# Optimization experiments

Measured on AMD Instinct MI355X. Metric: run time of the kernel, lower is better.

The kernel has to match this reference:

```python
import jax, jax.numpy as jnp
import numpy as np

N = 50000
E = 1600000
EPS = 1e-16


def transformer_conv(x, src, dst, ea, Wq, bq, Wk, bk, Wv, bv, We, Ws, bs):
    # PyG TransformerConv, heads=1, concat=True, root_weight=True
    C = Wq.shape[1]
    q = x @ Wq + bq                      # [N, C]
    k = x @ Wk + bk                      # [N, C]
    v = x @ Wv + bv                      # [N, C]
    e = ea @ We                          # [E, C]
    k_e = k[src] + e                     # per-edge key
    v_e = v[src] + e                     # per-edge value
    score = (q[dst] * k_e).sum(-1) / jnp.sqrt(jnp.asarray(C, x.dtype))  # [E]
    # segment softmax over incoming edges of each dst node
    m = jax.ops.segment_max(score, dst, num_segments=N)
    ex = jnp.exp(score - m[dst])
    denom = jax.ops.segment_sum(ex, dst, num_segments=N)
    alpha = ex / (denom[dst] + EPS)
    out = jax.ops.segment_sum(alpha[:, None] * v_e, dst, num_segments=N)
    return out + x @ Ws + bs             # skip connection


def gcn_conv(x, src, dst, W, b):
    # PyG GCNConv: self-loops + symmetric deg^-1/2 normalization
    n_idx = jnp.arange(N)
    src2 = jnp.concatenate([src, n_idx])
    dst2 = jnp.concatenate([dst, n_idx])
    deg = jax.ops.segment_sum(jnp.ones(E + N, x.dtype), dst2, num_segments=N)
    dinv = jnp.where(deg > 0, jax.lax.rsqrt(deg), 0.0)
    norm = dinv[src2] * dinv[dst2]       # [E+N]
    h = x @ W                            # [N, out]
    out = jax.ops.segment_sum(norm[:, None] * h[src2], dst2, num_segments=N)
    return out + b


def setup_inputs() -> dict:
    key = jax.random.key(0)
    ks = jax.random.split(key, 32)
    d = {}
    d['x'] = jax.random.normal(ks[0], (N, 128), jnp.float32)
    d['edge_index'] = jax.random.randint(ks[1], (2, E), 0, N, jnp.int64)
    d['edge_attr'] = jax.random.normal(ks[2], (E, 16), jnp.float32)
    shapes = dict(
        Wq1=(128, 96), bq1=(96,), Wk1=(128, 96), bk1=(96,), Wv1=(128, 96), bv1=(96,),
        We1=(16, 96), Ws1=(128, 96), bs1=(96,),
        Wq2=(96, 64), bq2=(64,), Wk2=(96, 64), bk2=(64,), Wv2=(96, 64), bv2=(64,),
        We2=(16, 64), Ws2=(96, 64), bs2=(64,),
        Wmu=(64, 32), bmu=(32,), Wls=(64, 32), bls=(32,))
    for i, (name, shp) in enumerate(shapes.items()):
        scale = 1.0 / np.sqrt(shp[0]) if len(shp) == 2 else 0.02
        d[name] = jax.random.normal(ks[3 + i], shp, jnp.float32) * scale
    return d


def reference(x, edge_index, edge_attr,
              Wq1, bq1, Wk1, bk1, Wv1, bv1, We1, Ws1, bs1,
              Wq2, bq2, Wk2, bk2, Wv2, bv2, We2, Ws2, bs2,
              Wmu, bmu, Wls, bls):
    src, dst = edge_index[0], edge_index[1]
    h = jax.nn.relu(transformer_conv(x, src, dst, edge_attr,
                                     Wq1, bq1, Wk1, bk1, Wv1, bv1, We1, Ws1, bs1))
    h = jax.nn.relu(transformer_conv(h, src, dst, edge_attr,
                                     Wq2, bq2, Wk2, bk2, Wv2, bv2, We2, Ws2, bs2))
    mu = gcn_conv(h, src, dst, Wmu, bmu)
    logstd = gcn_conv(h, src, dst, Wls, bls)
    return mu, logstd
```

## Files before the change

kernel.cpp:

```cpp
#include <hip/hip_runtime.h>
#include <math.h>


#define TPB 256
#define NGRP 8
typedef unsigned int uint32;
typedef unsigned long long u64;
typedef unsigned short u16;
typedef __attribute__((ext_vector_type(4))) float f32x4;
typedef __attribute__((ext_vector_type(4))) uint32 u32x4;
typedef __attribute__((ext_vector_type(4))) int i32x4;
typedef __attribute__((ext_vector_type(8))) short bf16x8;

__device__ __forceinline__ uint32 f2bf(float f) {
    uint32 u = __float_as_uint(f);
    return (u + 0x7fffu + ((u >> 16) & 1u)) >> 16;
}
__device__ __forceinline__ float bf2f(uint32 b) { return __uint_as_float(b << 16); }

__global__ void hist_kernel(const int* __restrict__ dst, int* __restrict__ deg,
                            int E, int span) {
    int grp = blockIdx.x & (NGRP - 1);
    int lo = grp * span;
    int nb = gridDim.x >> 3;
    int bid = blockIdx.x >> 3;
    int stride = nb * TPB * 8;
    for (int base = (bid * TPB + threadIdx.x) * 8; base < E; base += stride) {
        if (base + 8 <= E) {
            i32x4 d0 = __builtin_nontemporal_load((const i32x4*)(dst + base));
            i32x4 d1 = __builtin_nontemporal_load((const i32x4*)(dst + base + 4));
            int dv[8] = {d0.x, d0.y, d0.z, d0.w, d1.x, d1.y, d1.z, d1.w};
#pragma unroll
            for (int u = 0; u < 8; ++u)
                if ((uint32)(dv[u] - lo) < (uint32)span) atomicAdd(&deg[dv[u]], 1);
        } else {
            for (int i = base; i < E; ++i) {
                int d = dst[i];
                if ((uint32)(d - lo) < (uint32)span) atomicAdd(&deg[d], 1);
            }
        }
    }
}

__global__ __launch_bounds__(1024) void scan1_kernel(const int* __restrict__ deg,
                                                     int* __restrict__ prowp,
                                                     int* __restrict__ bsum, int n) {
    __shared__ int wsum[16];
    __shared__ int woff[16];
    int tid = threadIdx.x;
    int i = blockIdx.x * 1024 + tid;
    int lane = tid & 63, w = tid >> 6;
    int dg = (i < n) ? deg[i] : 0;
    int x = (dg + 7) & ~7;
    int v = x;
#pragma unroll
    for (int off = 1; off < 64; off <<= 1) {
        int t = __shfl_up(v, off, 64);
        if (lane >= off) v += t;
    }
    if (lane == 63) wsum[w] = v;
    __syncthreads();
    if (tid < 64) {
        int s = (tid < 16) ? wsum[tid] : 0;
#pragma unroll
        for (int off = 1; off < 16; off <<= 1) {
            int t = __shfl_up(s, off, 64);
            if (lane >= off) s += t;
        }
        if (tid < 16) woff[tid] = s;
    }
    __syncthreads();
    int incl = v + (w ? woff[w - 1] : 0);
    if (i < n) prowp[i] = incl;
    if (tid == 1023) bsum[blockIdx.x] = incl;
}

__global__ void scan2_kernel(const int* __restrict__ bsum, int* __restrict__ boff,
                             int* __restrict__ prowpN, int nb) {
    int tid = threadIdx.x;
    int x = (tid < nb) ? bsum[tid] : 0;
    int v = x;
#pragma unroll
    for (int off = 1; off < 64; off <<= 1) {
        int t = __shfl_up(v, off, 64);
        if (tid >= off) v += t;
    }
    if (tid < nb) boff[tid] = v - x;
    if (tid == nb - 1) *prowpN = v;
}

__global__ __launch_bounds__(1024) void scan3_kernel(const int* __restrict__ deg,
                                                     const int* __restrict__ boff,
                                                     int* __restrict__ prowp,
                                                     int* __restrict__ cursor,
                                                     float* __restrict__ dinv,
                                                     u64* __restrict__ pse, int n) {
    int i = blockIdx.x * 1024 + threadIdx.x;
    if (i < n) {
        int dg = deg[i];
        int x = (dg + 7) & ~7;
        int excl = prowp[i] - x + boff[blockIdx.x];
        prowp[i] = excl;
        cursor[i] = excl;
        dinv[i] = 1.0f / sqrtf((float)(dg + 1));
        u64 pad = (u64)(uint32)n;
        for (int p = excl + dg; p < excl + x; ++p) pse[p] = pad;
    }
}

__global__ void scatter_kernel(const int* __restrict__ src, const int* __restrict__ dst,
                               int* __restrict__ cursor, u64* __restrict__ pse,
                               int E, int span) {
    int grp = blockIdx.x & (NGRP - 1);
    int lo = grp * span;
    int nb = gridDim.x >> 3;
    int bid = blockIdx.x >> 3;
    int stride = nb * TPB * 8;
    for (int base = (bid * TPB + threadIdx.x) * 8; base < E; base += stride) {
        if (base + 8 <= E) {
            i32x4 d0 = __builtin_nontemporal_load((const i32x4*)(dst + base));
            i32x4 d1 = __builtin_nontemporal_load((const i32x4*)(dst + base + 4));
            i32x4 s0 = __builtin_nontemporal_load((const i32x4*)(src + base));
            i32x4 s1 = __builtin_nontemporal_load((const i32x4*)(src + base + 4));
            int dv[8] = {d0.x, d0.y, d0.z, d0.w, d1.x, d1.y, d1.z, d1.w};
            int sv[8] = {s0.x, s0.y, s0.z, s0.w, s1.x, s1.y, s1.z, s1.w};
#pragma unroll
            for (int u = 0; u < 8; ++u) {
                if ((uint32)(dv[u] - lo) < (uint32)span) {
                    int pos = atomicAdd(&cursor[dv[u]], 1);
                    pse[pos] = ((u64)(uint32)(base + u) << 32) | (uint32)sv[u];
                }
            }
        } else {
            for (int i = base; i < E; ++i) {
                int d = dst[i];
                if ((uint32)(d - lo) < (uint32)span) {
                    int pos = atomicAdd(&cursor[d], 1);
                    pse[pos] = ((u64)(uint32)i << 32) | (uint32)src[i];
                }
            }
        }
    }
}

__global__ void permute_kernel(const u64* __restrict__ pse, const float* __restrict__ EA,
                               const int* __restrict__ prowpN,
                               int* __restrict__ psrc, u16* __restrict__ EAb,
                               int N, int cap) {
    int i = blockIdx.x * TPB + threadIdx.x;
    if (i >= cap) return;
    int tot = *prowpN;
    if (i >= tot) return;
    u64 pk = __builtin_nontemporal_load(pse + i);
    uint32 s = (uint32)pk;
    uint32 eid = (uint32)(pk >> 32);
    __builtin_nontemporal_store((int)s, psrc + i);
    u32x4 lo = {0u, 0u, 0u, 0u}, hi = {0u, 0u, 0u, 0u};
    if (s != (uint32)N) {
        const f32x4* e4 = (const f32x4*)(EA + (size_t)eid * 16);
        f32x4 a = __builtin_nontemporal_load(e4);
        f32x4 b = __builtin_nontemporal_load(e4 + 1);
        f32x4 c = __builtin_nontemporal_load(e4 + 2);
        f32x4 d = __builtin_nontemporal_load(e4 + 3);
        lo = (u32x4){f2bf(a.x) | (f2bf(a.y) << 16), f2bf(a.z) | (f2bf(a.w) << 16),
                     f2bf(b.x) | (f2bf(b.y) << 16), f2bf(b.z) | (f2bf(b.w) << 16)};
        hi = (u32x4){f2bf(c.x) | (f2bf(c.y) << 16), f2bf(c.z) | (f2bf(c.w) << 16),
                     f2bf(d.x) | (f2bf(d.y) << 16), f2bf(d.z) | (f2bf(d.w) << 16)};
    }
    u32x4* o = (u32x4*)(EAb + (size_t)i * 16);
    __builtin_nontemporal_store(lo, o);
    __builtin_nontemporal_store(hi, o + 1);
}

__global__ void pack_kernel(
    const float* Wq1, const float* Wk1, const float* Wv1, const float* Ws1,
    const float* bq1, const float* bk1, const float* bv1, const float* bs1,
    const float* We1,
    const float* Wq2, const float* Wk2, const float* Wv2, const float* Ws2,
    const float* bq2, const float* bk2, const float* bv2, const float* bs2,
    const float* We2,
    const float* Wmu, const float* bmu, const float* Wls, const float* bls,
    const float* x, unsigned short* xb, int NX,
    unsigned short* Wc1t, float* bc1, unsigned short* Wc2t, float* bc2,
    float* Wc3, float* bc3) {
    const float s1 = 0.1020620726159658f;
    const float s2 = 0.125f;
    int gi = blockIdx.x * TPB + threadIdx.x;
    const int R0 = 448 * 128, R1 = R0 + 320 * 96, R2 = R1 + 64 * 64;
    const int R3 = R2 + 448, R4 = R3 + 320, R5 = R4 + 64;
    for (int i = gi; i < R5; i += gridDim.x * TPB) {
        if (i < R0) {
            int c = i / 128, kk = i % 128;
            float v = 0.f;
            if (c < 96) v = Wq1[kk * 96 + c] * s1;
            else if (c < 112) {
                int t = c - 96; float a = 0.f;
                for (int u = 0; u < 96; ++u) a += Wq1[kk * 96 + u] * We1[t * 96 + u];
                v = a * s1;
            } else if (c < 304) {
                int tt = c - 112;
                v = (tt & 1) ? Wv1[kk * 96 + (tt >> 1)] : Wk1[kk * 96 + (tt >> 1)];
            } else if (c < 400) v = Ws1[kk * 96 + (c - 304)];
            Wc1t[i] = (unsigned short)f2bf(v);
        } else if (i < R1) {
            int j = i - R0;
            int c = j / 96, kk = j % 96;
            float v = 0.f;
            if (c < 64) v = Wq2[kk * 64 + c] * s2;
            else if (c < 80) {
                int t = c - 64; float a = 0.f;
                for (int u = 0; u < 64; ++u) a += Wq2[kk * 64 + u] * We2[t * 64 + u];
                v = a * s2;
            } else if (c < 208) {
                int tt = c - 80;
                v = (tt & 1) ? Wv2[kk * 64 + (tt >> 1)] : Wk2[kk * 64 + (tt >> 1)];
            } else if (c < 272) v = Ws2[kk * 64 + (c - 208)];
            Wc2t[j] = (unsigned short)f2bf(v);
        } else if (i < R2) {
            int j = i - R1;
            int k = j / 64, c = j % 64;
            Wc3[j] = (c < 32) ? Wmu[k * 32 + c] : Wls[k * 32 + (c - 32)];
        } else if (i < R3) {
            int c = i - R2;
            float v = 0.f;
            if (c < 96) v = bq1[c] * s1;
            else if (c < 112) {
                int t = c - 96; float a = 0.f;
                for (int u = 0; u < 96; ++u) a += bq1[u] * We1[t * 96 + u];
                v = a * s1;
            } else if (c < 304) {
                int tt = c - 112;
                v = (tt & 1) ? bv1[tt >> 1] : bk1[tt >> 1];
            } else if (c < 400) v = bs1[c - 304];
            bc1[c] = v;
        } else if (i < R4) {
            int c = i - R3;
            float v = 0.f;
            if (c < 64) v = bq2[c] * s2;
            else if (c < 80) {
                int t = c - 64; float a = 0.f;
                for (int u = 0; u < 64; ++u) a += bq2[u] * We2[t * 64 + u];
                v = a * s2;
            } else if (c < 208) {
                int tt = c - 80;
                v = (tt & 1) ? bv2[tt >> 1] : bk2[tt >> 1];
            } else if (c < 272) v = bs2[c - 208];
            bc2[c] = v;
        } else {
            int c = i - R4;
            bc3[c] = (c < 32) ? bmu[c] : bls[c - 32];
        }
    }
    for (int i = gi; i < NX; i += gridDim.x * TPB)
        xb[i] = (unsigned short)f2bf(x[i]);
}

__global__ __launch_bounds__(256) void mfma_gemm_kernel(
    const unsigned short* __restrict__ A,
    const unsigned short* __restrict__ Wt,
    const float* __restrict__ bias,
    float* __restrict__ Qs, float* __restrict__ QE,
    uint32* __restrict__ KVp, float* __restrict__ SK,
    int N, int K, int Cq) {
    __shared__ unsigned short As[64][56];
    __shared__ unsigned short Bs[64][56];
    int r0 = blockIdx.x * 64, c0 = blockIdx.y * 64;
    int tid = threadIdx.x;
    int lane = tid & 63, w = tid >> 6;
    int wm = w >> 1, wn = w & 1;
    int l15 = lane & 15, l4 = lane >> 4;
    f32x4 zero = {0.f, 0.f, 0.f, 0.f};
    f32x4 acc[2][2] = {{zero, zero}, {zero, zero}};
    int sr = tid >> 2, sk = (tid & 3) * 8;

    for (int kc = 0; kc < K; kc += 32) {
        bf16x8 av = {};
        int ar = r0 + sr;
        if (ar < N) av = *(const bf16x8*)(A + (size_t)ar * K + kc + sk);
        *(bf16x8*)&As[sr][sk] = av;
        bf16x8 bv = *(const bf16x8*)(Wt + (size_t)(c0 + sr) * K + kc + sk);
        *(bf16x8*)&Bs[sr][sk] = bv;
        __syncthreads();
        bf16x8 af0 = *(const bf16x8*)&As[32 * wm + l15][l4 * 8];
        bf16x8 af1 = *(const bf16x8*)&As[32 * wm + 16 + l15][l4 * 8];
        bf16x8 bf0 = *(const bf16x8*)&Bs[32 * wn + l15][l4 * 8];
        bf16x8 bf1 = *(const bf16x8*)&Bs[32 * wn + 16 + l15][l4 * 8];
        acc[0][0] = __builtin_amdgcn_mfma_f32_16x16x32_bf16(af0, bf0, acc[0][0], 0, 0, 0);
        acc[0][1] = __builtin_amdgcn_mfma_f32_16x16x32_bf16(af0, bf1, acc[0][1], 0, 0, 0);
        acc[1][0] = __builtin_amdgcn_mfma_f32_16x16x32_bf16(af1, bf0, acc[1][0], 0, 0, 0);
        acc[1][1] = __builtin_amdgcn_mfma_f32_16x16x32_bf16(af1, bf1, acc[1][1], 0, 0, 0);
        __syncthreads();
    }

    int qe0 = Cq, kv0 = Cq + 16, sk0 = 3 * Cq + 16, end0 = 4 * Cq + 16;
#pragma unroll
    for (int fm = 0; fm < 2; ++fm) {
#pragma unroll
        for (int fn = 0; fn < 2; ++fn) {
            int cb = c0 + 32 * wn + 16 * fn;
            int c = cb + l15;
            float bia = bias[c];
#pragma unroll
            for (int r = 0; r < 4; ++r) {
                int row = r0 + 32 * wm + 16 * fm + l4 * 4 + r;
                float v = acc[fm][fn][r] + bia;
                float pv = __shfl_xor(v, 1, 64);
                bool ok = row < N;
                if (cb < qe0) {
                    if (ok) Qs[(size_t)row * Cq + c] = v;
                } else if (cb < kv0) {
                    if (ok) QE[(size_t)row * 16 + (c - qe0)] = v;
                } else if (cb < sk0) {
                    if (ok && !(l15 & 1)) {
                        int t = c - kv0;
                        KVp[(size_t)row * Cq + (t >> 1)] = (f2bf(v) << 16) | f2bf(pv);
                    }
                } else if (cb < end0) {
                    if (ok) SK[(size_t)row * Cq + (c - sk0)] = v;
                }
            }
        }
    }
}

template <int C>
__global__ __launch_bounds__(256) void edge_attn_kernel(
    const float* __restrict__ Qs, const float* __restrict__ SK,
    const uint32* __restrict__ KVp,
    const u16* __restrict__ EAb, const float* __restrict__ QE,
    const int* __restrict__ prowp, const int* __restrict__ deg,
    const int* __restrict__ psrc,
    float* __restrict__ Hpre, float* __restrict__ AEA, int N) {
    constexpr int CPL = C / 32;
    int n = blockIdx.x * 4 + (threadIdx.x >> 6);
    if (n >= N) return;
    int lane = threadIdx.x & 63;
    int half = lane >> 5, l = lane & 31, t16 = l & 15;
    bool lo16 = (l < 16);

    uint32 nC = (uint32)n * C;
    float q[CPL], acc[CPL];
#pragma unroll
    for (int j = 0; j < CPL; ++j) { q[j] = Qs[nC + l + 32 * j]; acc[j] = 0.f; }
    float qe = lo16 ? QE[(uint32)n * 16 + t16] : 0.f;
    float d = 0.f, aea = 0.f;
    int eb = prowp[n], ee = prowp[n + 1];

    for (int base = eb + 8 * half; base < ee; base += 16) {
        const int* sp = psrc + base;
        const u16* ep = EAb + (size_t)base * 16 + t16;
        float dots[8], eav[8];
        uint32 kv[8][CPL];
#pragma unroll
        for (int u = 0; u < 8; ++u) {
            int s = __builtin_nontemporal_load(sp + u);
            eav[u] = bf2f(__builtin_nontemporal_load(ep + u * 16));
            uint32 off = (uint32)s * C + l;
            float dt = qe * eav[u];
#pragma unroll
            for (int j = 0; j < CPL; ++j) {
                uint32 t = KVp[off + 32 * j];
                kv[u][j] = t;
                dt = fmaf(q[j], __uint_as_float(t & 0xffff0000u), dt);
            }
            dots[u] = dt;
        }
#pragma unroll
        for (int a = 0; a < 4; ++a) {
            float x0 = dots[2 * a], x1 = dots[2 * a + 1];
            float z = (lo16 ? x0 : x1) + __shfl_xor(lo16 ? x1 : x0, 16, 64);
            z += __shfl_xor(z, 8, 64);
            z += __shfl_xor(z, 4, 64);
            z += __shfl_xor(z, 2, 64);
            z += __shfl_xor(z, 1, 64);
            float p = __expf(z);
            float p0 = __shfl(p, 0, 32);
            float p1 = __shfl(p, 16, 32);
            d += p0 + p1;
            aea = fmaf(p0, eav[2 * a], fmaf(p1, eav[2 * a + 1], aea));
#pragma unroll
            for (int j = 0; j < CPL; ++j)
                acc[j] = fmaf(p0, __uint_as_float(kv[2 * a][j] << 16),
                         fmaf(p1, __uint_as_float(kv[2 * a + 1][j] << 16), acc[j]));
        }
    }
    d += __shfl_xor(d, 32, 64);
    aea += __shfl_xor(aea, 32, 64);
    d -= (float)((ee - eb) - deg[n]);
    float inv = 1.f / (d + 1e-16f);
#pragma unroll
    for (int j = 0; j < CPL; ++j) {
        float a2 = acc[j] + __shfl_xor(acc[j], 32, 64);
        if (half == 0)
            Hpre[nC + l + 32 * j] = a2 * inv + SK[nC + l + 32 * j];
    }
    if (lane < 16) AEA[(uint32)n * 16 + t16] = aea * inv;
}

template <int C>
__global__ void fixup_relu_kernel(const float* __restrict__ Hpre, const float* __restrict__ AEA,
                                  const float* __restrict__ We,
                                  unsigned short* __restrict__ H1b, int NC) {
    int idx = blockIdx.x * TPB + threadIdx.x;
    if (idx >= NC) return;
    int n = idx / C, c = idx % C;
    const float* a = AEA + (size_t)n * 16;
    float s = Hpre[idx];
#pragma unroll
    for (int t = 0; t < 16; ++t) s += a[t] * We[t * C + c];
    H1b[idx] = (unsigned short)f2bf(fmaxf(s, 0.f));
}

__global__ void fixup2_kernel(const float* __restrict__ Hpre, const float* __restrict__ AEA,
                              const float* __restrict__ We, const float* __restrict__ dinv,
                              uint32* __restrict__ H2p, int N) {
    int idx = blockIdx.x * TPB + threadIdx.x;
    if (idx >= N * 32) return;
    int n = idx >> 5, c = idx & 31;
    const float* a = AEA + (size_t)n * 16;
    float s0 = Hpre[(size_t)n * 64 + c];
    float s1 = Hpre[(size_t)n * 64 + 32 + c];
#pragma unroll
    for (int t = 0; t < 16; ++t) {
        s0 += a[t] * We[t * 64 + c];
        s1 += a[t] * We[t * 64 + 32 + c];
    }
    float dn = dinv[n];
    s0 = fmaxf(s0, 0.f) * dn;
    s1 = fmaxf(s1, 0.f) * dn;
    H2p[idx] = f2bf(s0) | (f2bf(s1) << 16);
}

__global__ __launch_bounds__(256) void gcn_agg_kernel(
    const uint32* __restrict__ H2p, const int* __restrict__ prowp,
    const int* __restrict__ psrc, const float* __restrict__ dinv,
    float* __restrict__ AGG, int N) {
    int n = blockIdx.x * 4 + (threadIdx.x >> 6);
    if (n >= N) return;
    int lane = threadIdx.x & 63, half = lane >> 5, l = lane & 31;
    float s0 = 0.f, s1 = 0.f;
    int eb = prowp[n], ee = prowp[n + 1];
    for (int base = eb + 8 * half; base < ee; base += 16) {
        const int* sp = psrc + base;
#pragma unroll
        for (int u = 0; u < 8; ++u) {
            uint32 s = (uint32)__builtin_nontemporal_load(sp + u);
            uint32 t = H2p[s * 32 + l];
            s0 += bf2f(t & 0xffffu);
            s1 += __uint_as_float(t & 0xffff0000u);
        }
    }
    s0 += __shfl_xor(s0, 32, 64);
    s1 += __shfl_xor(s1, 32, 64);
    if (half == 0) {
        uint32 u = H2p[(uint32)n * 32 + l];
        float dn = dinv[n];
        AGG[(uint32)n * 64 + l]      = dn * (s0 + bf2f(u & 0xffffu));
        AGG[(uint32)n * 64 + 32 + l] = dn * (s1 + __uint_as_float(u & 0xffff0000u));
    }
}

template <int CT, bool SPLIT>
__global__ __launch_bounds__(256) void gemm_kernel(
    const float* __restrict__ A, const float* __restrict__ W,
    const float* __restrict__ bias, float* __restrict__ Out,
    float* __restrict__ Out2, int N, int K, int C) {
    constexpr int TC = CT / 16;
    __shared__ float As[32][68];
    __shared__ float Bs[32][CT + 4];
    int r0 = blockIdx.x * 64, c0 = blockIdx.y * CT;
    int t = threadIdx.x;
    int tr = t >> 4, tc = t & 15;
    float acc[4][TC];
#pragma unroll
    for (int i = 0; i < 4; ++i)
#pragma unroll
        for (int j = 0; j < TC; ++j) acc[i][j] = 0.f;

    for (int kc = 0; kc < K; kc += 32) {
        int ra = t >> 2, kq = (t & 3) * 8;
        float4 a0 = {0, 0, 0, 0}, a1 = {0, 0, 0, 0};
        int r = r0 + ra;
        if (r < N) {
            const float* ap = A + (size_t)r * K + kc + kq;
            a0 = *(const float4*)ap;
            a1 = *(const float4*)(ap + 4);
        }
        As[kq + 0][ra] = a0.x; As[kq + 1][ra] = a0.y;
        As[kq + 2][ra] = a0.z; As[kq + 3][ra] = a0.w;
        As[kq + 4][ra] = a1.x; As[kq + 5][ra] = a1.y;
        As[kq + 6][ra] = a1.z; As[kq + 7][ra] = a1.w;
        constexpr int PASSES = (32 * CT) / (256 * 8);
#pragma unroll
        for (int p = 0; p < PASSES; ++p) {
            int idx = (t + p * 256) * 8;
            int k = idx / CT, c = idx % CT;
            const float* wp = W + (size_t)(kc + k) * C + c0 + c;
            float4 b0 = *(const float4*)wp;
            float4 b1 = *(const float4*)(wp + 4);
            *(float4*)&Bs[k][c] = b0;
            *(float4*)&Bs[k][c + 4] = b1;
        }
        __syncthreads();
#pragma unroll
        for (int k = 0; k < 32; ++k) {
            float4 av = *(const float4*)&As[k][tr * 4];
            float a[4] = {av.x, av.y, av.z, av.w};
#pragma unroll
            for (int u = 0; u < TC / 4; ++u) {
                float4 bv = *(const float4*)&Bs[k][tc * TC + u * 4];
                float b[4] = {bv.x, bv.y, bv.z, bv.w};
#pragma unroll
                for (int i = 0; i < 4; ++i)
#pragma unroll
                    for (int j = 0; j < 4; ++j) acc[i][u * 4 + j] += a[i] * b[j];
            }
        }
        __syncthreads();
    }
#pragma unroll
    for (int i = 0; i < 4; ++i) {
        int r = r0 + tr * 4 + i;
        if (r >= N) continue;
#pragma unroll
        for (int j = 0; j < TC; ++j) {
            int c = c0 + tc * TC + j;
            float v = acc[i][j] + bias[c];
            if (SPLIT) {
                if (c < 32) Out[(size_t)r * 32 + c] = v;
                else        Out2[(size_t)r * 32 + c - 32] = v;
            } else {
                Out[(size_t)r * C + c] = v;
            }
        }
    }
}

extern "C" void kernel_launch(void* const* d_in, const int* in_sizes, int n_in,
                              void* d_out, int out_size, void* d_ws, size_t ws_size,
                              hipStream_t stream) {
    const float* x   = (const float*)d_in[0];
    const int*   ei  = (const int*)d_in[1];
    const float* ea  = (const float*)d_in[2];
    const float* Wq1 = (const float*)d_in[3];  const float* bq1 = (const float*)d_in[4];
    const float* Wk1 = (const float*)d_in[5];  const float* bk1 = (const float*)d_in[6];
    const float* Wv1 = (const float*)d_in[7];  const float* bv1 = (const float*)d_in[8];
    const float* We1 = (const float*)d_in[9];
    const float* Ws1 = (const float*)d_in[10]; const float* bs1 = (const float*)d_in[11];
    const float* Wq2 = (const float*)d_in[12]; const float* bq2 = (const float*)d_in[13];
    const float* Wk2 = (const float*)d_in[14]; const float* bk2 = (const float*)d_in[15];
    const float* Wv2 = (const float*)d_in[16]; const float* bv2 = (const float*)d_in[17];
    const float* We2 = (const float*)d_in[18];
    const float* Ws2 = (const float*)d_in[19]; const float* bs2 = (const float*)d_in[20];
    const float* Wmu = (const float*)d_in[21]; const float* bmu = (const float*)d_in[22];
    const float* Wls = (const float*)d_in[23]; const float* bls = (const float*)d_in[24];

    int N = in_sizes[0] / 128;
    int E = in_sizes[1] / 2;
    const int* src = ei;
    const int* dst = ei + E;
    int E2max = E + 8 * N;
    int span = (N + NGRP - 1) / NGRP;

    char* ws = (char*)d_ws;
    size_t off = 0;
    auto alloc = [&](size_t bytes) -> char* {
        char* p = ws + off;
        off = (off + bytes + 255) & ~(size_t)255;
        return p;
    };
    int*      deg    = (int*)alloc((size_t)N * 4);
    int*      prowp  = (int*)alloc((size_t)(N + 1) * 4);
    int*      cursor = (int*)alloc((size_t)N * 4);
    float*    dinv   = (float*)alloc((size_t)N * 4);
    int*      bsum   = (int*)alloc(256 * 4);
    int*      boff   = (int*)alloc(256 * 4);
    u64*      pse    = (u64*)alloc((size_t)E2max * 8);
    int*      psrc   = (int*)alloc((size_t)E2max * 4);
    u16*      EAb    = (u16*)alloc((size_t)E2max * 16 * 2);
    unsigned short* Wc1t = (unsigned short*)alloc(448 * 128 * 2);
    float*    bc1    = (float*)alloc(448 * 4);
    unsigned short* Wc2t = (unsigned short*)alloc(320 * 96 * 2);
    float*    bc2    = (float*)alloc(320 * 4);
    float*    Wc3    = (float*)alloc(64 * 64 * 4);
    float*    bc3    = (float*)alloc(64 * 4);
    unsigned short* xb = (unsigned short*)alloc((size_t)N * 128 * 2);
    float*    Qs   = (float*)alloc((size_t)N * 96 * 4);
    float*    QE   = (float*)alloc((size_t)N * 16 * 4);
    uint32*   KVp  = (uint32*)alloc((size_t)(N + 1) * 96 * 4);
    float*    SKb  = (float*)alloc((size_t)N * 96 * 4);
    float*    Hpre = (float*)alloc((size_t)N * 96 * 4);
    unsigned short* H1b = (unsigned short*)alloc((size_t)N * 96 * 2);
    float*    AEA  = (float*)alloc((size_t)N * 16 * 4);
    uint32*   H2p  = (uint32*)alloc((size_t)(N + 1) * 32 * 4);
    float*    AGG  = (float*)alloc((size_t)N * 64 * 4);

    (void)hipMemsetAsync(deg, 0, (size_t)N * 4, stream);
    (void)hipMemsetAsync(KVp + (size_t)N * 96, 0, 96 * 4, stream);
    (void)hipMemsetAsync(H2p + (size_t)N * 32, 0, 32 * 4, stream);

    int e2bk = (E2max + TPB - 1) / TPB;
    int nb1k = (N + 1023) / 1024;
    hist_kernel<<<2048, TPB, 0, stream>>>(dst, deg, E, span);
    scan1_kernel<<<nb1k, 1024, 0, stream>>>(deg, prowp, bsum, N);
    scan2_kernel<<<1, 64, 0, stream>>>(bsum, boff, prowp + N, nb1k);
    scan3_kernel<<<nb1k, 1024, 0, stream>>>(deg, boff, prowp, cursor, dinv, pse, N);
    scatter_kernel<<<2048, TPB, 0, stream>>>(src, dst, cursor, pse, E, span);
    permute_kernel<<<e2bk, TPB, 0, stream>>>(pse, ea, prowp + N, psrc, EAb, N, E2max);
    pack_kernel<<<364, TPB, 0, stream>>>(Wq1, Wk1, Wv1, Ws1, bq1, bk1, bv1, bs1, We1,
                                         Wq2, Wk2, Wv2, Ws2, bq2, bk2, bv2, bs2, We2,
                                         Wmu, bmu, Wls, bls, x, xb, N * 128,
                                         Wc1t, bc1, Wc2t, bc2, Wc3, bc3);

    int rb = (N + 63) / 64;
    int nb4 = (N + 3) / 4;

    mfma_gemm_kernel<<<dim3(rb, 7), 256, 0, stream>>>(xb, Wc1t, bc1, Qs, QE, KVp, SKb,
                                                      N, 128, 96);
    edge_attn_kernel<96><<<nb4, 256, 0, stream>>>(Qs, SKb, KVp, EAb, QE, prowp, deg, psrc,
                                                  Hpre, AEA, N);
    fixup_relu_kernel<96><<<(N * 96 + TPB - 1) / TPB, TPB, 0, stream>>>(Hpre, AEA, We1,
                                                                        H1b, N * 96);
    mfma_gemm_kernel<<<dim3(rb, 5), 256, 0, stream>>>(H1b, Wc2t, bc2, Qs, QE, KVp, SKb,
                                                      N, 96, 64);
    (void)hipMemsetAsync(KVp + (size_t)N * 64, 0, 64 * 4, stream);
    edge_attn_kernel<64><<<nb4, 256, 0, stream>>>(Qs, SKb, KVp, EAb, QE, prowp, deg, psrc,
                                                  Hpre, AEA, N);
    fixup2_kernel<<<(N * 32 + TPB - 1) / TPB, TPB, 0, stream>>>(Hpre, AEA, We2, dinv, H2p, N);
    gcn_agg_kernel<<<nb4, 256, 0, stream>>>(H2p, prowp, psrc, dinv, AGG, N);
    gemm_kernel<64, true><<<dim3(rb, 1), 256, 0, stream>>>(AGG, Wc3, bc3, (float*)d_out,
                                                           (float*)d_out + (size_t)N * 32,
                                                           N, 64, 64);
}
```

Baseline: 567.6 us.

## Fuse fixup/ReLU epilogues into edge attention and pack Q with skip as bf16

Interleaves the query and skip-connection weight columns so the GEMM writes one packed bf16 pair per channel instead of two separate fp32 arrays. The edge attention kernel now applies the edge-attribute correction (aea·We), ReLU, bf16 conversion and the GCN dinv scaling directly in its epilogue. This removes the separate fixup kernels and the Hpre/AEA/SK intermediate round-trips through global memory. In exchange, Q and the skip term are stored at bf16 precision, and the epilogue adds 16 shuffles plus We loads per channel.

```diff
diff --git a/kernel.cpp b/kernel.cpp
--- a/kernel.cpp
+++ b/kernel.cpp
@@ -192,29 +192,33 @@
         if (i < R0) {
             int c = i / 128, kk = i % 128;
             float v = 0.f;
-            if (c < 96) v = Wq1[kk * 96 + c] * s1;
-            else if (c < 112) {
-                int t = c - 96; float a = 0.f;
+            if (c < 192) {
+                int ch = c >> 1;
+                v = (c & 1) ? Ws1[kk * 96 + ch] : Wq1[kk * 96 + ch] * s1;
+            } else if (c < 208) {
+                int t = c - 192; float a = 0.f;
                 for (int u = 0; u < 96; ++u) a += Wq1[kk * 96 + u] * We1[t * 96 + u];
                 v = a * s1;
-            } else if (c < 304) {
-                int tt = c - 112;
+            } else if (c < 400) {
+                int tt = c - 208;
                 v = (tt & 1) ? Wv1[kk * 96 + (tt >> 1)] : Wk1[kk * 96 + (tt >> 1)];
-            } else if (c < 400) v = Ws1[kk * 96 + (c - 304)];
+            }
             Wc1t[i] = (unsigned short)f2bf(v);
         } else if (i < R1) {
             int j = i - R0;
             int c = j / 96, kk = j % 96;
             float v = 0.f;
-            if (c < 64) v = Wq2[kk * 64 + c] * s2;
-            else if (c < 80) {
-                int t = c - 64; float a = 0.f;
+            if (c < 128) {
+                int ch = c >> 1;
+                v = (c & 1) ? Ws2[kk * 64 + ch] : Wq2[kk * 64 + ch] * s2;
+            } else if (c < 144) {
+                int t = c - 128; float a = 0.f;
                 for (int u = 0; u < 64; ++u) a += Wq2[kk * 64 + u] * We2[t * 64 + u];
                 v = a * s2;
-            } else if (c < 208) {
-                int tt = c - 80;
+            } else if (c < 272) {
+                int tt = c - 144;
                 v = (tt & 1) ? Wv2[kk * 64 + (tt >> 1)] : Wk2[kk * 64 + (tt >> 1)];
-            } else if (c < 272) v = Ws2[kk * 64 + (c - 208)];
+            }
             Wc2t[j] = (unsigned short)f2bf(v);
         } else if (i < R2) {
             int j = i - R1;
@@ -223,28 +227,32 @@
         } else if (i < R3) {
             int c = i - R2;
             float v = 0.f;
-            if (c < 96) v = bq1[c] * s1;
-            else if (c < 112) {
-                int t = c - 96; float a = 0.f;
+            if (c < 192) {
+                int ch = c >> 1;
+                v = (c & 1) ? bs1[ch] : bq1[ch] * s1;
+            } else if (c < 208) {
+                int t = c - 192; float a = 0.f;
                 for (int u = 0; u < 96; ++u) a += bq1[u] * We1[t * 96 + u];
                 v = a * s1;
-            } else if (c < 304) {
-                int tt = c - 112;
+            } else if (c < 400) {
+                int tt = c - 208;
                 v = (tt & 1) ? bv1[tt >> 1] : bk1[tt >> 1];
-            } else if (c < 400) v = bs1[c - 304];
+            }
             bc1[c] = v;
         } else if (i < R4) {
             int c = i - R3;
             float v = 0.f;
-            if (c < 64) v = bq2[c] * s2;
-            else if (c < 80) {
-                int t = c - 64; float a = 0.f;
+            if (c < 128) {
+                int ch = c >> 1;
+                v = (c & 1) ? bs2[ch] : bq2[ch] * s2;
+            } else if (c < 144) {
+                int t = c - 128; float a = 0.f;
                 for (int u = 0; u < 64; ++u) a += bq2[u] * We2[t * 64 + u];
                 v = a * s2;
-            } else if (c < 208) {
-                int tt = c - 80;
+            } else if (c < 272) {
+                int tt = c - 144;
                 v = (tt & 1) ? bv2[tt >> 1] : bk2[tt >> 1];
-            } else if (c < 272) v = bs2[c - 208];
+            }
             bc2[c] = v;
         } else {
             int c = i - R4;
@@ -259,8 +267,8 @@
     const unsigned short* __restrict__ A,
     const unsigned short* __restrict__ Wt,
     const float* __restrict__ bias,
-    float* __restrict__ Qs, float* __restrict__ QE,
-    uint32* __restrict__ KVp, float* __restrict__ SK,
+    uint32* __restrict__ QSp, float* __restrict__ QE,
+    uint32* __restrict__ KVp,
     int N, int K, int Cq) {
     __shared__ unsigned short As[64][56];
     __shared__ unsigned short Bs[64][56];
@@ -292,7 +300,7 @@
         __syncthreads();
     }
 
-    int qe0 = Cq, kv0 = Cq + 16, sk0 = 3 * Cq + 16, end0 = 4 * Cq + 16;
+    int qs0 = 2 * Cq, qe1 = 2 * Cq + 16, kv1 = 4 * Cq + 16;
 #pragma unroll
     for (int fm = 0; fm < 2; ++fm) {
 #pragma unroll
@@ -305,18 +313,16 @@
                 int row = r0 + 32 * wm + 16 * fm + l4 * 4 + r;
                 float v = acc[fm][fn][r] + bia;
                 float pv = __shfl_xor(v, 1, 64);
-                bool ok = row < N;
-                if (cb < qe0) {
-                    if (ok) Qs[(size_t)row * Cq + c] = v;
-                } else if (cb < kv0) {
-                    if (ok) QE[(size_t)row * 16 + (c - qe0)] = v;
-                } else if (cb < sk0) {
-                    if (ok && !(l15 & 1)) {
-                        int t = c - kv0;
+                bool ok = (row < N) && !(l15 & 1);
+                if (cb < qs0) {
+                    if (ok) QSp[(size_t)row * Cq + (c >> 1)] = (f2bf(v) << 16) | f2bf(pv);
+                } else if (cb < qe1) {
+                    if (row < N) QE[(size_t)row * 16 + (c - qs0)] = v;
+                } else if (cb < kv1) {
+                    if (ok) {
+                        int t = c - qe1;
                         KVp[(size_t)row * Cq + (t >> 1)] = (f2bf(v) << 16) | f2bf(pv);
                     }
-                } else if (cb < end0) {
-                    if (ok) SK[(size_t)row * Cq + (c - sk0)] = v;
                 }
             }
         }
@@ -325,12 +331,12 @@
 
 template <int C>
 __global__ __launch_bounds__(256) void edge_attn_kernel(
-    const float* __restrict__ Qs, const float* __restrict__ SK,
-    const uint32* __restrict__ KVp,
+    const uint32* __restrict__ QSp, const uint32* __restrict__ KVp,
     const u16* __restrict__ EAb, const float* __restrict__ QE,
     const int* __restrict__ prowp, const int* __restrict__ deg,
-    const int* __restrict__ psrc,
-    float* __restrict__ Hpre, float* __restrict__ AEA, int N) {
+    const int* __restrict__ psrc, const float* __restrict__ We,
+    const float* __restrict__ dinv,
+    unsigned short* __restrict__ H1b, uint32* __restrict__ H2p, int N) {
     constexpr int CPL = C / 32;
     int n = blockIdx.x * 4 + (threadIdx.x >> 6);
     if (n >= N) return;
@@ -339,9 +345,14 @@
     bool lo16 = (l < 16);
 
     uint32 nC = (uint32)n * C;
-    float q[CPL], acc[CPL];
-#pragma unroll
-    for (int j = 0; j < CPL; ++j) { q[j] = Qs[nC + l + 32 * j]; acc[j] = 0.f; }
+    float q[CPL], skv[CPL], acc[CPL];
+#pragma unroll
+    for (int j = 0; j < CPL; ++j) {
+        uint32 u = QSp[nC + l + 32 * j];
+        q[j] = __uint_as_float(u & 0xffff0000u);
+        skv[j] = bf2f(u & 0xffffu);
+        acc[j] = 0.f;
+    }
     float qe = lo16 ? QE[(uint32)n * 16 + t16] : 0.f;
     float d = 0.f, aea = 0.f;
     int eb = prowp[n], ee = prowp[n + 1];
@@ -388,47 +399,28 @@
     aea += __shfl_xor(aea, 32, 64);
     d -= (float)((ee - eb) - deg[n]);
     float inv = 1.f / (d + 1e-16f);
+    float aeaF = aea * inv;
+
+    float h[CPL];
 #pragma unroll
     for (int j = 0; j < CPL; ++j) {
-        float a2 = acc[j] + __shfl_xor(acc[j], 32, 64);
-        if (half == 0)
-            Hpre[nC + l + 32 * j] = a2 * inv + SK[nC + l + 32 * j];
-    }
-    if (lane < 16) AEA[(uint32)n * 16 + t16] = aea * inv;
-}
-
-template <int C>
-__global__ void fixup_relu_kernel(const float* __restrict__ Hpre, const float* __restrict__ AEA,
-                                  const float* __restrict__ We,
-                                  unsigned short* __restrict__ H1b, int NC) {
-    int idx = blockIdx.x * TPB + threadIdx.x;
-    if (idx >= NC) return;
-    int n = idx / C, c = idx % C;
-    const float* a = AEA + (size_t)n * 16;
-    float s = Hpre[idx];
-#pragma unroll
-    for (int t = 0; t < 16; ++t) s += a[t] * We[t * C + c];
-    H1b[idx] = (unsigned short)f2bf(fmaxf(s, 0.f));
-}
-
-__global__ void fixup2_kernel(const float* __restrict__ Hpre, const float* __restrict__ AEA,
-                              const float* __restrict__ We, const float* __restrict__ dinv,
-                              uint32* __restrict__ H2p, int N) {
-    int idx = blockIdx.x * TPB + threadIdx.x;
-    if (idx >= N * 32) return;
-    int n = idx >> 5, c = idx & 31;
-    const float* a = AEA + (size_t)n * 16;
-    float s0 = Hpre[(size_t)n * 64 + c];
-    float s1 = Hpre[(size_t)n * 64 + 32 + c];
-#pragma unroll
-    for (int t = 0; t < 16; ++t) {
-        s0 += a[t] * We[t * 64 + c];
-        s1 += a[t] * We[t * 64 + 32 + c];
-    }
-    float dn = dinv[n];
-    s0 = fmaxf(s0, 0.f) * dn;
-    s1 = fmaxf(s1, 0.f) * dn;
-    H2p[idx] = f2bf(s0) | (f2bf(s1) << 16);
+        float s = fmaf(acc[j] + __shfl_xor(acc[j], 32, 64), inv, skv[j]);
+        int c = l + 32 * j;
+#pragma unroll
+        for (int t = 0; t < 16; ++t)
+            s = fmaf(__shfl(aeaF, t, 64), We[t * C + c], s);
+        h[j] = fmaxf(s, 0.f);
+    }
+    if (half == 0) {
+        if (C == 96) {
+#pragma unroll
+            for (int j = 0; j < CPL; ++j)
+                H1b[nC + l + 32 * j] = (unsigned short)f2bf(h[j]);
+        } else {
+            float dn = dinv[n];
+            H2p[(uint32)n * 32 + l] = f2bf(h[0] * dn) | (f2bf(h[1] * dn) << 16);
+        }
+    }
 }
 
 __global__ __launch_bounds__(256) void gcn_agg_kernel(
@@ -585,13 +577,10 @@
     float*    Wc3    = (float*)alloc(64 * 64 * 4);
     float*    bc3    = (float*)alloc(64 * 4);
     unsigned short* xb = (unsigned short*)alloc((size_t)N * 128 * 2);
-    float*    Qs   = (float*)alloc((size_t)N * 96 * 4);
+    uint32*   QSp  = (uint32*)alloc((size_t)N * 96 * 4);
     float*    QE   = (float*)alloc((size_t)N * 16 * 4);
     uint32*   KVp  = (uint32*)alloc((size_t)(N + 1) * 96 * 4);
-    float*    SKb  = (float*)alloc((size_t)N * 96 * 4);
-    float*    Hpre = (float*)alloc((size_t)N * 96 * 4);
     unsigned short* H1b = (unsigned short*)alloc((size_t)N * 96 * 2);
-    float*    AEA  = (float*)alloc((size_t)N * 16 * 4);
     uint32*   H2p  = (uint32*)alloc((size_t)(N + 1) * 32 * 4);
     float*    AGG  = (float*)alloc((size_t)N * 64 * 4);
 
@@ -615,18 +604,15 @@
     int rb = (N + 63) / 64;
     int nb4 = (N + 3) / 4;
 
-    mfma_gemm_kernel<<<dim3(rb, 7), 256, 0, stream>>>(xb, Wc1t, bc1, Qs, QE, KVp, SKb,
+    mfma_gemm_kernel<<<dim3(rb, 7), 256, 0, stream>>>(xb, Wc1t, bc1, QSp, QE, KVp,
                                                       N, 128, 96);
-    edge_attn_kernel<96><<<nb4, 256, 0, stream>>>(Qs, SKb, KVp, EAb, QE, prowp, deg, psrc,
-                                                  Hpre, AEA, N);
-    fixup_relu_kernel<96><<<(N * 96 + TPB - 1) / TPB, TPB, 0, stream>>>(Hpre, AEA, We1,
-                                                                        H1b, N * 96);
-    mfma_gemm_kernel<<<dim3(rb, 5), 256, 0, stream>>>(H1b, Wc2t, bc2, Qs, QE, KVp, SKb,
+    edge_attn_kernel<96><<<nb4, 256, 0, stream>>>(QSp, KVp, EAb, QE, prowp, deg, psrc,
+                                                  We1, dinv, H1b, nullptr, N);
+    mfma_gemm_kernel<<<dim3(rb, 5), 256, 0, stream>>>(H1b, Wc2t, bc2, QSp, QE, KVp,
                                                       N, 96, 64);
     (void)hipMemsetAsync(KVp + (size_t)N * 64, 0, 64 * 4, stream);
-    edge_attn_kernel<64><<<nb4, 256, 0, stream>>>(Qs, SKb, KVp, EAb, QE, prowp, deg, psrc,
-                                                  Hpre, AEA, N);
-    fixup2_kernel<<<(N * 32 + TPB - 1) / TPB, TPB, 0, stream>>>(Hpre, AEA, We2, dinv, H2p, N);
+    edge_attn_kernel<64><<<nb4, 256, 0, stream>>>(QSp, KVp, EAb, QE, prowp, deg, psrc,
+                                                  We2, dinv, nullptr, H2p, N);
     gcn_agg_kernel<<<nb4, 256, 0, stream>>>(H2p, prowp, psrc, dinv, AGG, N);
     gemm_kernel<64, true><<<dim3(rb, 1), 256, 0, stream>>>(AGG, Wc3, bc3, (float*)d_out,
                                                            (float*)d_out + (size_t)N * 32,
```

New measurement: 536.3 us. 1.06x faster.
